# Optimization experiments

Measured on AMD Instinct MI355X. Metric: run time of the kernel, lower is better.

The kernel has to match this reference:

```python
import jax, jax.numpy as jnp
import numpy as np

B = 64        # number of queries (eg_idx)
E = 1024      # edges per query (contiguous blocks)
N = B * E     # total edges
M = 65536     # number of visited nodes
D = 128       # n_dims_in
D4 = 4 * D    # G3 concat dim


def setup_inputs():
    key = jax.random.key(0)
    ks = jax.random.split(key, 12)
    std = np.sqrt(2.0 / D4).astype(np.float32)
    visited_node_score = jax.random.uniform(ks[0], (M,), dtype=jnp.float32)
    visited_node_representation = jax.random.normal(ks[1], (M, D), dtype=jnp.float32)
    rel_emb = jax.random.normal(ks[2], (N, D), dtype=jnp.float32)
    query_src_ts_emb = jax.random.normal(ks[3], (B, D), dtype=jnp.float32)
    query_rel_emb = jax.random.normal(ks[4], (B, D), dtype=jnp.float32)
    Wq = jax.random.normal(ks[5], (D4, D4), dtype=jnp.float32) * std
    Wk = jax.random.normal(ks[6], (D4, D4), dtype=jnp.float32) * std
    # edges: (eg_idx, vi, ti, vj, tj, rel, node_idx_i, node_idx_j)
    eg_idx = jnp.repeat(jnp.arange(B, dtype=jnp.int32), E)          # sorted by query
    node_i = jnp.sort(jax.random.randint(ks[7], (N,), 0, M, dtype=jnp.int32))  # contiguous segments
    node_j = jax.random.randint(ks[8], (N,), 0, M, dtype=jnp.int32)
    dummy = jax.random.randint(ks[9], (N, 4), 0, M, dtype=jnp.int32)
    edges = jnp.concatenate([eg_idx[:, None], dummy[:, :3], dummy[:, 3:4],
                             jnp.zeros((N, 1), jnp.int32), node_i[:, None], node_j[:, None]], axis=1)
    return {
        'visited_node_score': visited_node_score,
        'visited_node_representation': visited_node_representation,
        'rel_emb': rel_emb,
        'query_src_ts_emb': query_src_ts_emb,
        'query_rel_emb': query_rel_emb,
        'Wq': Wq,
        'Wk': Wk,
        'edges': edges,
        'max_edges': 64,
    }


def _attention_flow(visited_node_score, visited_node_representation, rel_emb,
                    query_src_ts_emb, query_rel_emb, Wq, Wk, edges, max_edges):
    seg = edges[:, 6]            # node_idx_i: segment ids (contiguous blocks)
    eg = edges[:, 0]             # query index
    hvi = visited_node_representation[seg]           # [N, D]
    hvj = visited_node_representation[edges[:, 7]]   # [N, D]
    qs = query_src_ts_emb[eg]                        # [N, D]
    qr = query_rel_emb[eg]                           # [N, D]
    left = jnp.concatenate([hvi, rel_emb, qs, qr], axis=-1)   # [N, 4D]
    right = jnp.concatenate([hvj, rel_emb, qs, qr], axis=-1)  # [N, 4D]
    # G3 bilinear score: sum(query_proj(left) * key_proj(right), -1)
    logits = jnp.sum((left @ Wq.T) * (right @ Wk.T), axis=-1)  # [N]
    # segment softmax over node_idx_i segments
    smax = jax.ops.segment_max(logits, seg, num_segments=M)
    ex = jnp.exp(logits - smax[seg])
    den = jax.ops.segment_sum(ex, seg, num_segments=M)
    soft = ex / den[seg]                                       # [N]
    src_score = visited_node_score[seg]
    target_score = soft * src_score                            # [N]
    # per-query top-k pruning (edges are contiguous per query)
    vals, idx = jax.lax.top_k(target_score.reshape(B, E), max_edges)  # [B, k]
    orig_indices = (idx + jnp.arange(B, dtype=idx.dtype)[:, None] * E).reshape(-1)
    pruned_target_score = vals.reshape(-1)
    pruned_softmax = soft[orig_indices]
    pruned_edges = edges[orig_indices]
    return pruned_target_score, pruned_softmax, pruned_edges, orig_indices


def reference(visited_node_score, visited_node_representation, rel_emb,
              query_src_ts_emb, query_rel_emb, Wq, Wk, edges, max_edges):
    return _attention_flow(visited_node_score, visited_node_representation, rel_emb,
                           query_src_ts_emb, query_rel_emb, Wq, Wk, edges, max_edges)
```

## Files before the change

### kernel.cpp

```cpp
#include <hip/hip_runtime.h>
#include <math.h>

#define MM 65536
#define NN 65536
#define BBATCH 64
#define EPB 1024
#define DD 128
#define KTOP 64

__global__ void k_gemm_G(const float* __restrict__ Wq, const float* __restrict__ Wk,
                         float* __restrict__ G)
{
    __shared__ float As[32][33];
    __shared__ float Bs[32][33];
    const int t  = threadIdx.x;
    const int tm = t >> 4, tn = t & 15;
    const int m0 = (blockIdx.x >> 4) * 32, n0 = (blockIdx.x & 15) * 32;
    float a00 = 0.f, a01 = 0.f, a10 = 0.f, a11 = 0.f;
    for (int d0 = 0; d0 < 512; d0 += 32) {
        for (int i = t; i < 1024; i += 256) {
            int r = i >> 5, c = i & 31;
            As[r][c] = Wq[(size_t)(d0 + r) * 512 + m0 + c];
            Bs[r][c] = Wk[(size_t)(d0 + r) * 512 + n0 + c];
        }
        __syncthreads();
        #pragma unroll 8
        for (int k = 0; k < 32; ++k) {
            float x0 = As[k][tm * 2], x1 = As[k][tm * 2 + 1];
            float y0 = Bs[k][tn * 2], y1 = Bs[k][tn * 2 + 1];
            a00 += x0 * y0; a01 += x0 * y1; a10 += x1 * y0; a11 += x1 * y1;
        }
        __syncthreads();
    }
    G[(size_t)(m0 + tm * 2 + 0) * 512 + n0 + tn * 2 + 0] = a00;
    G[(size_t)(m0 + tm * 2 + 0) * 512 + n0 + tn * 2 + 1] = a01;
    G[(size_t)(m0 + tm * 2 + 1) * 512 + n0 + tn * 2 + 0] = a10;
    G[(size_t)(m0 + tm * 2 + 1) * 512 + n0 + tn * 2 + 1] = a11;
}

__global__ void k_batch(const float* __restrict__ qs, const float* __restrict__ qr,
                        const float* __restrict__ G,
                        float* __restrict__ bL, float* __restrict__ bR, float* __restrict__ cB)
{
    const int e = blockIdx.x, t = threadIdx.x;
    __shared__ float qcat[256];
    __shared__ float whi[256];
    __shared__ float red[256];
    qcat[t] = (t < 128) ? qs[(size_t)e * 128 + t] : qr[(size_t)e * 128 + (t - 128)];
    __syncthreads();
    float w0 = 0.f, w1 = 0.f;
    for (int r = 0; r < 256; ++r) {
        float q = qcat[r];
        w0 += G[(size_t)t * 512 + 256 + r] * q;
        w1 += G[(size_t)(t + 256) * 512 + 256 + r] * q;
    }
    bL[(size_t)e * 256 + t] = w0;
    whi[t] = w1;
    float v = 0.f;
    for (int r = 0; r < 256; ++r)
        v += qcat[r] * G[(size_t)(256 + r) * 512 + t];
    bR[(size_t)e * 256 + t] = v;
    __syncthreads();
    red[t] = qcat[t] * whi[t];
    __syncthreads();
    for (int s = 128; s > 0; s >>= 1) {
        if (t < s) red[t] += red[t + s];
        __syncthreads();
    }
    if (t == 0) cB[e] = red[0];
}

__launch_bounds__(256, 2)
__global__ void k_edge(const float* __restrict__ vnr, const float* __restrict__ rel,
                       const int* __restrict__ edges, const float* __restrict__ G,
                       const float* __restrict__ bL, const float* __restrict__ bR,
                       const float* __restrict__ cB, float* __restrict__ logits)
{
    __shared__ float At[128][64];
    __shared__ float Bt[128][64];
    __shared__ int   segL[64], jL[64];
    __shared__ float bLs[256], bRs[256];

    const int t  = threadIdx.x;
    const int n0 = blockIdx.x * 64;
    const int eg = n0 >> 10;

    if (t < 64) {
        segL[t] = edges[(size_t)(n0 + t) * 8 + 6];
        jL[t]   = edges[(size_t)(n0 + t) * 8 + 7];
    }
    bLs[t] = bL[(size_t)eg * 256 + t];
    bRs[t] = bR[(size_t)eg * 256 + t];

    const int g = t & 7, p = t >> 3;
    const int e0 = 2 * p, e1 = 2 * p + 1;
    const int eS = t & 63, rep = t >> 6;

    double s0 = 0.0, s1 = 0.0;

    for (int kt = 0; kt < 2; ++kt) {
        __syncthreads();
        {
            const float* src = (kt == 0) ? (vnr + (size_t)segL[eS] * 128)
                                         : (rel + (size_t)(n0 + eS) * 128);
            #pragma unroll
            for (int w = 0; w < 8; ++w) {
                int k = rep * 32 + w * 4;
                float4 v = *(const float4*)(src + k);
                At[k + 0][eS] = v.x; At[k + 1][eS] = v.y;
                At[k + 2][eS] = v.z; At[k + 3][eS] = v.w;
            }
        }
        __syncthreads();
        {
            float a0 = 0.f, a1 = 0.f;
            #pragma unroll
            for (int kk = 0; kk < 16; ++kk) {
                int k = g * 16 + kk;
                float bl = bLs[kt * 128 + k];
                a0 += At[k][e0] * bl;
                a1 += At[k][e1] * bl;
            }
            s0 += (double)a0; s1 += (double)a1;
        }
        for (int ct = 0; ct < 4; ++ct) {
            __syncthreads();
            {
                int kk = t >> 1, half = t & 1;
                const float* gsrc = G + (size_t)(kt * 128 + kk) * 512 + ct * 64 + half * 32;
                #pragma unroll
                for (int w = 0; w < 8; ++w) {
                    int c  = half * 32 + w * 4;
                    int cs = c ^ ((kk & 7) << 3);
                    *(float4*)&Bt[kk][cs] = *(const float4*)(gsrc + w * 4);
                }
            }
            __syncthreads();
            float acc0[8] = {0.f,0.f,0.f,0.f,0.f,0.f,0.f,0.f};
            float acc1[8] = {0.f,0.f,0.f,0.f,0.f,0.f,0.f,0.f};
            #pragma unroll 4
            for (int kk = 0; kk < 128; ++kk) {
                const float2 a = *(const float2*)&At[kk][e0];
                const int cb = (g * 8) ^ ((kk & 7) << 3);
                const float4 b0 = *(const float4*)&Bt[kk][cb];
                const float4 b1 = *(const float4*)&Bt[kk][cb + 4];
                acc0[0] += a.x * b0.x; acc0[1] += a.x * b0.y;
                acc0[2] += a.x * b0.z; acc0[3] += a.x * b0.w;
                acc0[4] += a.x * b1.x; acc0[5] += a.x * b1.y;
                acc0[6] += a.x * b1.z; acc0[7] += a.x * b1.w;
                acc1[0] += a.y * b0.x; acc1[1] += a.y * b0.y;
                acc1[2] += a.y * b0.z; acc1[3] += a.y * b0.w;
                acc1[4] += a.y * b1.x; acc1[5] += a.y * b1.y;
                acc1[6] += a.y * b1.z; acc1[7] += a.y * b1.w;
            }
            const float* r0p; const float* r1p;
            if (ct < 2) {
                r0p = vnr + (size_t)jL[e0] * 128 + ct * 64 + g * 8;
                r1p = vnr + (size_t)jL[e1] * 128 + ct * 64 + g * 8;
            } else {
                r0p = rel + (size_t)(n0 + e0) * 128 + (ct - 2) * 64 + g * 8;
                r1p = rel + (size_t)(n0 + e1) * 128 + (ct - 2) * 64 + g * 8;
            }
            const float4 ra = *(const float4*)r0p, rb = *(const float4*)(r0p + 4);
            const float4 rc = *(const float4*)r1p, rd = *(const float4*)(r1p + 4);
            float d0 = acc0[0]*ra.x + acc0[1]*ra.y + acc0[2]*ra.z + acc0[3]*ra.w
                     + acc0[4]*rb.x + acc0[5]*rb.y + acc0[6]*rb.z + acc0[7]*rb.w;
            float d1 = acc1[0]*rc.x + acc1[1]*rc.y + acc1[2]*rc.z + acc1[3]*rc.w
                     + acc1[4]*rd.x + acc1[5]*rd.y + acc1[6]*rd.z + acc1[7]*rd.w;
            s0 += (double)d0; s1 += (double)d1;
            if (kt == 0) {
                const int cb = ct * 64 + g * 8;
                float q0 = ra.x*bRs[cb+0] + ra.y*bRs[cb+1] + ra.z*bRs[cb+2] + ra.w*bRs[cb+3]
                         + rb.x*bRs[cb+4] + rb.y*bRs[cb+5] + rb.z*bRs[cb+6] + rb.w*bRs[cb+7];
                float q1 = rc.x*bRs[cb+0] + rc.y*bRs[cb+1] + rc.z*bRs[cb+2] + rc.w*bRs[cb+3]
                         + rd.x*bRs[cb+4] + rd.y*bRs[cb+5] + rd.z*bRs[cb+6] + rd.w*bRs[cb+7];
                s0 += (double)q0; s1 += (double)q1;
            }
        }
    }
    #pragma unroll
    for (int m = 1; m < 8; m <<= 1) {
        s0 += __shfl_xor(s0, m, 64);
        s1 += __shfl_xor(s1, m, 64);
    }
    if (g == 0) {
        float base = cB[eg];
        logits[n0 + e0] = (float)s0 + base;
        logits[n0 + e1] = (float)s1 + base;
    }
}

__global__ void k_segstats(const int* __restrict__ edges, const float* __restrict__ logits,
                           float* __restrict__ smaxf, float* __restrict__ den)
{
    int n = blockIdx.x * 256 + threadIdx.x;
    if (n >= NN) return;
    int s = edges[(size_t)n * 8 + 6];
    if (n > 0 && edges[(size_t)(n - 1) * 8 + 6] == s) return;
    float m = -INFINITY;
    int k = n;
    while (k < NN && edges[(size_t)k * 8 + 6] == s) {
        m = fmaxf(m, logits[k]);
        ++k;
    }
    float d = 0.f;
    for (int q = n; q < k; ++q) d += expf(logits[q] - m);
    smaxf[s] = m;
    den[s]   = d;
}

__global__ void k_topk(const int* __restrict__ edges, const float* __restrict__ logits,
                       const float* __restrict__ smaxf, const float* __restrict__ den,
                       const float* __restrict__ score, float* __restrict__ out)
{
    __shared__ float vals[1024];
    __shared__ int   idxs[1024];
    const int r = blockIdx.x, t = threadIdx.x;
    const int n = r * 1024 + t;
    {
        int s = edges[(size_t)n * 8 + 6];
        float soft = expf(logits[n] - smaxf[s]) / den[s];
        vals[t] = soft * score[s];
        idxs[t] = t;
    }
    __syncthreads();
    for (int size = 2; size <= 1024; size <<= 1) {
        for (int stride = size >> 1; stride > 0; stride >>= 1) {
            int j = t ^ stride;
            if (j > t) {
                float v1 = vals[t], v2 = vals[j];
                int   i1 = idxs[t], i2 = idxs[j];
                bool before = (v1 > v2) || (v1 == v2 && i1 < i2);
                bool desc   = ((t & size) == 0);
                if (before != desc) {
                    vals[t] = v2; vals[j] = v1;
                    idxs[t] = i2; idxs[j] = i1;
                }
            }
            __syncthreads();
        }
    }
    if (t < KTOP) {
        int idx  = idxs[t];
        int orig = r * 1024 + idx;
        int s    = edges[(size_t)orig * 8 + 6];
        float soft = expf(logits[orig] - smaxf[s]) / den[s];
        int o = r * KTOP + t;
        out[o]            = vals[t];
        out[4096 + o]     = soft;
        #pragma unroll
        for (int q = 0; q < 8; ++q)
            out[8192 + (size_t)o * 8 + q] = (float)edges[(size_t)orig * 8 + q];
        out[40960 + o]    = (float)orig;
    }
}

extern "C" void kernel_launch(void* const* d_in, const int* in_sizes, int n_in,
                              void* d_out, int out_size, void* d_ws, size_t ws_size,
                              hipStream_t stream)
{
    (void)in_sizes; (void)n_in; (void)out_size; (void)ws_size;
    const float* score = (const float*)d_in[0];
    const float* vnr   = (const float*)d_in[1];
    const float* rel   = (const float*)d_in[2];
    const float* qs    = (const float*)d_in[3];
    const float* qr    = (const float*)d_in[4];
    const float* Wq    = (const float*)d_in[5];
    const float* Wk    = (const float*)d_in[6];
    const int*   edges = (const int*)  d_in[7];
    float* out = (float*)d_out;

    float* ws     = (float*)d_ws;
    float* G      = ws;
    float* bL     = G      + 262144;
    float* bR     = bL     + 16384;
    float* cB     = bR     + 16384;
    float* smaxf  = cB     + 64;
    float* den    = smaxf  + 65536;
    float* logits = den    + 65536;

    k_gemm_G <<<256, 256, 0, stream>>>(Wq, Wk, G);
    k_batch  <<<64, 256, 0, stream>>>(qs, qr, G, bL, bR, cB);
    k_edge   <<<1024, 256, 0, stream>>>(vnr, rel, edges, G, bL, bR, cB, logits);
    k_segstats<<<256, 256, 0, stream>>>(edges, logits, smaxf, den);
    k_topk   <<<64, 1024, 0, stream>>>(edges, logits, smaxf, den, score, out);
}
```

Baseline: 326.7 us.

## Retile edge kernel with 4x8 register tiles, prefetching, and shuffle-based bitonic top-k

The edge bilinear kernel now gives each thread 4 edges by 8 columns over half the k-range, instead of 2 edges over the full range. This raises register reuse of the shared-memory loads. The next G tile and the rel/vnr rows are prefetched into registers while the current tile is being computed, which cuts the number of barriers and hides global load latency. The top-k bitonic sort keeps values in registers and uses wavefront shuffles for strides under 64, so it drops most shared-memory traffic and __syncthreads calls. The risks are higher register pressure under launch_bounds(256,2) and an extra cross-lane reduction step.

```diff
diff --git a/kernel.cpp b/kernel.cpp
--- a/kernel.cpp
+++ b/kernel.cpp
@@ -3,9 +3,6 @@
 
 #define MM 65536
 #define NN 65536
-#define BBATCH 64
-#define EPB 1024
-#define DD 128
 #define KTOP 64
 
 __global__ void k_gemm_G(const float* __restrict__ Wq, const float* __restrict__ Wk,
@@ -70,123 +67,150 @@
     if (t == 0) cB[e] = red[0];
 }
 
+#define FMAROW(J, AX) \
+    acc[J][0] += AX * b0.x; acc[J][1] += AX * b0.y; \
+    acc[J][2] += AX * b0.z; acc[J][3] += AX * b0.w; \
+    acc[J][4] += AX * b1.x; acc[J][5] += AX * b1.y; \
+    acc[J][6] += AX * b1.z; acc[J][7] += AX * b1.w;
+
 __launch_bounds__(256, 2)
 __global__ void k_edge(const float* __restrict__ vnr, const float* __restrict__ rel,
                        const int* __restrict__ edges, const float* __restrict__ G,
                        const float* __restrict__ bL, const float* __restrict__ bR,
                        const float* __restrict__ cB, float* __restrict__ logits)
 {
-    __shared__ float At[128][64];
-    __shared__ float Bt[128][64];
-    __shared__ int   segL[64], jL[64];
-    __shared__ float bLs[256], bRs[256];
+    __shared__ __align__(16) float At[128][64];
+    __shared__ __align__(16) float Bt[128][64];
+    __shared__ __align__(16) float bLs[256];
+    __shared__ __align__(16) float bRs[256];
+    __shared__ int jL[64];
 
     const int t  = threadIdx.x;
     const int n0 = blockIdx.x * 64;
     const int eg = n0 >> 10;
 
-    if (t < 64) {
-        segL[t] = edges[(size_t)(n0 + t) * 8 + 6];
-        jL[t]   = edges[(size_t)(n0 + t) * 8 + 7];
-    }
+    const int kh = t & 1;
+    const int g  = (t >> 1) & 7;
+    const int p  = t >> 4;
+    const int e0 = p * 4;
+    const int eS = t & 63, rep = t >> 6;
+    const int kk2 = t >> 1, half = t & 1;
+
+    if (t < 64) jL[t] = edges[(size_t)(n0 + t) * 8 + 7];
     bLs[t] = bL[(size_t)eg * 256 + t];
     bRs[t] = bR[(size_t)eg * 256 + t];
 
-    const int g = t & 7, p = t >> 3;
-    const int e0 = 2 * p, e1 = 2 * p + 1;
-    const int eS = t & 63, rep = t >> 6;
-
-    double s0 = 0.0, s1 = 0.0;
+    float4 apre[8], gpre[8];
+    {
+        int segMine = edges[(size_t)(n0 + eS) * 8 + 6];
+        const float* asrc = vnr + (size_t)segMine * 128 + rep * 32;
+        #pragma unroll
+        for (int w = 0; w < 8; ++w) apre[w] = *(const float4*)(asrc + w * 4);
+        const float* gsrc = G + (size_t)kk2 * 512 + half * 32;
+        #pragma unroll
+        for (int w = 0; w < 8; ++w) gpre[w] = *(const float4*)(gsrc + w * 4);
+    }
+    __syncthreads();
+
+    double s[4] = {0.0, 0.0, 0.0, 0.0};
 
     for (int kt = 0; kt < 2; ++kt) {
+        if (kt > 0) __syncthreads();
+        #pragma unroll
+        for (int w = 0; w < 8; ++w) {
+            int k = rep * 32 + w * 4;
+            At[k + 0][eS] = apre[w].x; At[k + 1][eS] = apre[w].y;
+            At[k + 2][eS] = apre[w].z; At[k + 3][eS] = apre[w].w;
+        }
         __syncthreads();
+        if (kt == 0) {
+            const float* asrc = rel + (size_t)(n0 + eS) * 128 + rep * 32;
+            #pragma unroll
+            for (int w = 0; w < 8; ++w) apre[w] = *(const float4*)(asrc + w * 4);
+        }
         {
-            const float* src = (kt == 0) ? (vnr + (size_t)segL[eS] * 128)
-                                         : (rel + (size_t)(n0 + eS) * 128);
-            #pragma unroll
-            for (int w = 0; w < 8; ++w) {
-                int k = rep * 32 + w * 4;
-                float4 v = *(const float4*)(src + k);
-                At[k + 0][eS] = v.x; At[k + 1][eS] = v.y;
-                At[k + 2][eS] = v.z; At[k + 3][eS] = v.w;
-            }
-        }
-        __syncthreads();
-        {
-            float a0 = 0.f, a1 = 0.f;
-            #pragma unroll
-            for (int kk = 0; kk < 16; ++kk) {
-                int k = g * 16 + kk;
+            float la[4] = {0.f, 0.f, 0.f, 0.f};
+            const int kb = (t & 15) * 8;
+            #pragma unroll
+            for (int i = 0; i < 8; ++i) {
+                int k = kb + i;
                 float bl = bLs[kt * 128 + k];
-                a0 += At[k][e0] * bl;
-                a1 += At[k][e1] * bl;
-            }
-            s0 += (double)a0; s1 += (double)a1;
-        }
+                float4 a = *(const float4*)&At[k][e0];
+                la[0] += a.x * bl; la[1] += a.y * bl;
+                la[2] += a.z * bl; la[3] += a.w * bl;
+            }
+            #pragma unroll
+            for (int j = 0; j < 4; ++j) s[j] += (double)la[j];
+        }
+
         for (int ct = 0; ct < 4; ++ct) {
-            __syncthreads();
+            const int tt = kt * 4 + ct;
+            if (ct > 0) __syncthreads();
             {
-                int kk = t >> 1, half = t & 1;
-                const float* gsrc = G + (size_t)(kt * 128 + kk) * 512 + ct * 64 + half * 32;
+                const int swz = ((kk2 & 7) << 3) ^ (((kk2 >> 6) & 1) << 2);
                 #pragma unroll
                 for (int w = 0; w < 8; ++w) {
                     int c  = half * 32 + w * 4;
-                    int cs = c ^ ((kk & 7) << 3);
-                    *(float4*)&Bt[kk][cs] = *(const float4*)(gsrc + w * 4);
+                    *(float4*)&Bt[kk2][c ^ swz] = gpre[w];
                 }
             }
             __syncthreads();
-            float acc0[8] = {0.f,0.f,0.f,0.f,0.f,0.f,0.f,0.f};
-            float acc1[8] = {0.f,0.f,0.f,0.f,0.f,0.f,0.f,0.f};
-            #pragma unroll 4
-            for (int kk = 0; kk < 128; ++kk) {
-                const float2 a = *(const float2*)&At[kk][e0];
-                const int cb = (g * 8) ^ ((kk & 7) << 3);
-                const float4 b0 = *(const float4*)&Bt[kk][cb];
-                const float4 b1 = *(const float4*)&Bt[kk][cb + 4];
-                acc0[0] += a.x * b0.x; acc0[1] += a.x * b0.y;
-                acc0[2] += a.x * b0.z; acc0[3] += a.x * b0.w;
-                acc0[4] += a.x * b1.x; acc0[5] += a.x * b1.y;
-                acc0[6] += a.x * b1.z; acc0[7] += a.x * b1.w;
-                acc1[0] += a.y * b0.x; acc1[1] += a.y * b0.y;
-                acc1[2] += a.y * b0.z; acc1[3] += a.y * b0.w;
-                acc1[4] += a.y * b1.x; acc1[5] += a.y * b1.y;
-                acc1[6] += a.y * b1.z; acc1[7] += a.y * b1.w;
-            }
-            const float* r0p; const float* r1p;
-            if (ct < 2) {
-                r0p = vnr + (size_t)jL[e0] * 128 + ct * 64 + g * 8;
-                r1p = vnr + (size_t)jL[e1] * 128 + ct * 64 + g * 8;
-            } else {
-                r0p = rel + (size_t)(n0 + e0) * 128 + (ct - 2) * 64 + g * 8;
-                r1p = rel + (size_t)(n0 + e1) * 128 + (ct - 2) * 64 + g * 8;
-            }
-            const float4 ra = *(const float4*)r0p, rb = *(const float4*)(r0p + 4);
-            const float4 rc = *(const float4*)r1p, rd = *(const float4*)(r1p + 4);
-            float d0 = acc0[0]*ra.x + acc0[1]*ra.y + acc0[2]*ra.z + acc0[3]*ra.w
-                     + acc0[4]*rb.x + acc0[5]*rb.y + acc0[6]*rb.z + acc0[7]*rb.w;
-            float d1 = acc1[0]*rc.x + acc1[1]*rc.y + acc1[2]*rc.z + acc1[3]*rc.w
-                     + acc1[4]*rd.x + acc1[5]*rd.y + acc1[6]*rd.z + acc1[7]*rd.w;
-            s0 += (double)d0; s1 += (double)d1;
-            if (kt == 0) {
-                const int cb = ct * 64 + g * 8;
-                float q0 = ra.x*bRs[cb+0] + ra.y*bRs[cb+1] + ra.z*bRs[cb+2] + ra.w*bRs[cb+3]
-                         + rb.x*bRs[cb+4] + rb.y*bRs[cb+5] + rb.z*bRs[cb+6] + rb.w*bRs[cb+7];
-                float q1 = rc.x*bRs[cb+0] + rc.y*bRs[cb+1] + rc.z*bRs[cb+2] + rc.w*bRs[cb+3]
-                         + rd.x*bRs[cb+4] + rd.y*bRs[cb+5] + rd.z*bRs[cb+6] + rd.w*bRs[cb+7];
-                s0 += (double)q0; s1 += (double)q1;
+            if (tt < 7) {
+                const int ntt = tt + 1, nkt = ntt >> 2, nct = ntt & 3;
+                const float* gsrc = G + (size_t)(nkt * 128 + kk2) * 512 + nct * 64 + half * 32;
+                #pragma unroll
+                for (int w = 0; w < 8; ++w) gpre[w] = *(const float4*)(gsrc + w * 4);
+            }
+            float4 rpre[8];
+            #pragma unroll
+            for (int j = 0; j < 4; ++j) {
+                const float* rp = (ct < 2)
+                    ? (vnr + (size_t)jL[e0 + j] * 128 + ct * 64 + g * 8)
+                    : (rel + (size_t)(n0 + e0 + j) * 128 + (ct - 2) * 64 + g * 8);
+                rpre[2 * j]     = *(const float4*)(rp);
+                rpre[2 * j + 1] = *(const float4*)(rp + 4);
+            }
+            float acc[4][8] = {};
+            const int cb0 = (g * 8) ^ (kh << 2);
+            #pragma unroll 8
+            for (int i = 0; i < 64; ++i) {
+                const int kk = kh * 64 + i;
+                float4 a  = *(const float4*)&At[kk][e0];
+                const int cb = cb0 ^ ((i & 7) << 3);
+                float4 b0 = *(const float4*)&Bt[kk][cb];
+                float4 b1 = *(const float4*)&Bt[kk][cb ^ 4];
+                FMAROW(0, a.x) FMAROW(1, a.y) FMAROW(2, a.z) FMAROW(3, a.w)
+            }
+            const int cbase = ct * 64 + g * 8;
+            const bool doBR = (kt == 0) && (kh == 0);
+            float4 br0, br1;
+            if (doBR) {
+                br0 = *(const float4*)&bRs[cbase];
+                br1 = *(const float4*)&bRs[cbase + 4];
+            }
+            #pragma unroll
+            for (int j = 0; j < 4; ++j) {
+                float4 ra = rpre[2 * j], rb = rpre[2 * j + 1];
+                float d = acc[j][0] * ra.x + acc[j][1] * ra.y + acc[j][2] * ra.z + acc[j][3] * ra.w
+                        + acc[j][4] * rb.x + acc[j][5] * rb.y + acc[j][6] * rb.z + acc[j][7] * rb.w;
+                if (doBR) {
+                    d += ra.x * br0.x + ra.y * br0.y + ra.z * br0.z + ra.w * br0.w
+                       + rb.x * br1.x + rb.y * br1.y + rb.z * br1.z + rb.w * br1.w;
+                }
+                s[j] += (double)d;
             }
         }
     }
     #pragma unroll
-    for (int m = 1; m < 8; m <<= 1) {
-        s0 += __shfl_xor(s0, m, 64);
-        s1 += __shfl_xor(s1, m, 64);
-    }
-    if (g == 0) {
+    for (int m = 1; m < 16; m <<= 1) {
+        #pragma unroll
+        for (int j = 0; j < 4; ++j) s[j] += __shfl_xor(s[j], m, 64);
+    }
+    if ((t & 15) == 0) {
         float base = cB[eg];
-        logits[n0 + e0] = (float)s0 + base;
-        logits[n0 + e1] = (float)s1 + base;
+        #pragma unroll
+        for (int j = 0; j < 4; ++j)
+            logits[n0 + e0 + j] = (float)s[j] + base;
     }
 }
 
@@ -213,45 +237,44 @@
                        const float* __restrict__ smaxf, const float* __restrict__ den,
                        const float* __restrict__ score, float* __restrict__ out)
 {
-    __shared__ float vals[1024];
-    __shared__ int   idxs[1024];
+    __shared__ float vsh[1024];
+    __shared__ int   ish[1024];
     const int r = blockIdx.x, t = threadIdx.x;
     const int n = r * 1024 + t;
+    float v; int idx = t;
     {
         int s = edges[(size_t)n * 8 + 6];
-        float soft = expf(logits[n] - smaxf[s]) / den[s];
-        vals[t] = soft * score[s];
-        idxs[t] = t;
-    }
-    __syncthreads();
+        v = expf(logits[n] - smaxf[s]) / den[s] * score[s];
+    }
     for (int size = 2; size <= 1024; size <<= 1) {
         for (int stride = size >> 1; stride > 0; stride >>= 1) {
-            int j = t ^ stride;
-            if (j > t) {
-                float v1 = vals[t], v2 = vals[j];
-                int   i1 = idxs[t], i2 = idxs[j];
-                bool before = (v1 > v2) || (v1 == v2 && i1 < i2);
-                bool desc   = ((t & size) == 0);
-                if (before != desc) {
-                    vals[t] = v2; vals[j] = v1;
-                    idxs[t] = i2; idxs[j] = i1;
-                }
-            }
-            __syncthreads();
+            float v2; int i2;
+            if (stride < 64) {
+                v2 = __shfl_xor(v, stride, 64);
+                i2 = __shfl_xor(idx, stride, 64);
+            } else {
+                __syncthreads();
+                vsh[t] = v; ish[t] = idx;
+                __syncthreads();
+                v2 = vsh[t ^ stride]; i2 = ish[t ^ stride];
+            }
+            bool before = (v > v2) || (v == v2 && idx < i2);
+            bool desc   = ((t & size) == 0);
+            bool keep   = ((t & stride) == 0) ? (before == desc) : (before != desc);
+            if (!keep) { v = v2; idx = i2; }
         }
     }
     if (t < KTOP) {
-        int idx  = idxs[t];
         int orig = r * 1024 + idx;
-        int s    = edges[(size_t)orig * 8 + 6];
-        float soft = expf(logits[orig] - smaxf[s]) / den[s];
+        int ss   = edges[(size_t)orig * 8 + 6];
+        float soft = expf(logits[orig] - smaxf[ss]) / den[ss];
         int o = r * KTOP + t;
-        out[o]            = vals[t];
-        out[4096 + o]     = soft;
+        out[o]        = v;
+        out[4096 + o] = soft;
         #pragma unroll
         for (int q = 0; q < 8; ++q)
             out[8192 + (size_t)o * 8 + q] = (float)edges[(size_t)orig * 8 + q];
-        out[40960 + o]    = (float)orig;
+        out[40960 + o] = (float)orig;
     }
 }
 
@@ -279,9 +302,9 @@
     float* den    = smaxf  + 65536;
     float* logits = den    + 65536;
 
-    k_gemm_G <<<256, 256, 0, stream>>>(Wq, Wk, G);
-    k_batch  <<<64, 256, 0, stream>>>(qs, qr, G, bL, bR, cB);
-    k_edge   <<<1024, 256, 0, stream>>>(vnr, rel, edges, G, bL, bR, cB, logits);
+    k_gemm_G  <<<256, 256, 0, stream>>>(Wq, Wk, G);
+    k_batch   <<<64, 256, 0, stream>>>(qs, qr, G, bL, bR, cB);
+    k_edge    <<<1024, 256, 0, stream>>>(vnr, rel, edges, G, bL, bR, cB, logits);
     k_segstats<<<256, 256, 0, stream>>>(edges, logits, smaxf, den);
-    k_topk   <<<64, 1024, 0, stream>>>(edges, logits, smaxf, den, score, out);
-}
+    k_topk    <<<64, 1024, 0, stream>>>(edges, logits, smaxf, den, score, out);
+}
```

New measurement: 397.0 us. 21.5% more time.
